# Kernel tuning notes

Hardware: AMD Instinct MI355X
Metric: run time of the kernel (lower is better)

Reference implementation:

```python
import jax, jax.numpy as jnp
import numpy as np

# Dimensions (see shape_source): B batches, W walks, L walk length, N anonymized node-id space
B, W, L, N = 256, 128, 20, 64
SIGMA = 2.0  # CooccurrenceMatrix(sigma=2.0)


def setup_inputs() -> dict:
    key = jax.random.key(0)
    k1, k2 = jax.random.split(key)
    anonymized_nodes = jax.random.randint(k1, (B, W, L), 0, N, dtype=jnp.int32)
    walk_masks = jax.random.randint(k2, (B, W, L), 0, 2).astype(bool)
    # Gaussian positional kernel buffer: kernel[i,j] = exp(-(i-j)^2 / sigma^2)
    pos = jnp.arange(L, dtype=jnp.float32)
    kernel = jnp.exp(-((pos[:, None] - pos[None, :]) ** 2) / (SIGMA ** 2))
    return {"anonymized_nodes": anonymized_nodes, "walk_masks": walk_masks, "kernel": kernel}


def reference(anonymized_nodes, walk_masks, kernel):
    # Faithful vectorized form of CooccurrenceMatrix.forward.
    # Original: per batch, group valid (walk,pos) entries by node id (sort +
    # change-points); for each group with >=2 entries, scatter-add
    # kernel[pos_i, pos_j] into cooccurrence[b, walk_i, walk_j] for all pairs
    # (i,j) in the group (including i==j). Then normalize by outer product of
    # walk lengths, clamp, tanh.
    valid = walk_masks.astype(jnp.float32)                     # [B,W,L]
    # T[b,w,l,n] = 1 if entry (w,l) is valid and holds node id n
    T = jax.nn.one_hot(anonymized_nodes, N, dtype=jnp.float32) * valid[..., None]  # [B,W,L,N]
    # Segments with < 2 occurrences contribute nothing (original skips them)
    cnt = T.sum(axis=(1, 2))                                   # [B,N]
    T = T * (cnt >= 2.0).astype(jnp.float32)[:, None, None, :]
    K = jnp.clip(kernel, -10.0, 10.0)                          # clamp as in _add_segment_deterministic
    # cooccurrence[b,w,v] = sum_n sum_{l,m} T[b,w,l,n] K[l,m] T[b,v,m,n]
    S = jnp.einsum('bwln,lm->bwmn', T, K)                      # [B,W,L,N]
    cooc = jnp.einsum('bwmn,bvmn->bwv', S, T)                  # [B,W,W]
    # Normalization by walk-length outer product
    walk_lens = valid.sum(-1)                                  # [B,W]
    norm = jnp.clip(walk_lens[:, :, None] * walk_lens[:, None, :], 1e-6, None)
    valid_pairs = (walk_lens[:, :, None] > 0) & (walk_lens[:, None, :] > 0)
    cooc = jnp.where(valid_pairs, cooc / norm, 0.0)
    return jnp.tanh(jnp.clip(cooc, -10.0, 10.0))
```

## Files before the change

### kernel.cpp

```cpp
#include <hip/hip_runtime.h>
#include <hip/hip_bf16.h>

#define BB   256
#define W    128
#define L    20
#define NN   64
#define WL   (W * L)
#define NT   1024
#define CS   129
#define NSLOT 3
#define ENTPAD 8192

__global__ __launch_bounds__(NT) void cooc_kernel(
    const int* __restrict__ nodes,
    const void* __restrict__ masks,
    const float* __restrict__ kern,
    float* __restrict__ out)
{
    __shared__ __align__(16) float cooc[W * CS];
    __shared__ unsigned short ent[WL + ENTPAD];
    __shared__ int cnt[NN];
    __shared__ int cur[NN];
    __shared__ int eIncl[NN];
    __shared__ int wlen[W];
    __shared__ int det[3];

    const int tid = threadIdx.x;
    const int b = blockIdx.x;
    const int base = b * WL;

    const unsigned mword = ((const unsigned*)masks)[tid];
    int nval[NSLOT];
    #pragma unroll
    for (int k = 0; k < NSLOT; k++) {
        int e = tid + k * NT;
        nval[k] = (e < WL) ? nodes[base + e] : 0;
    }

    if (tid < 3) det[tid] = 0;
    if (tid < NN) cnt[tid] = 0;
    if (tid < W) wlen[tid] = 0;
    {
        float4* c4 = (float4*)cooc;
        for (int i = tid; i < (W * CS) / 4; i += NT)
            c4[i] = make_float4(0.f, 0.f, 0.f, 0.f);
    }
    {
        unsigned v = mword;
        unsigned long long b0 = __ballot(v > 1u);
        unsigned long long b1 = __ballot(v != 0u && v != 0x3F800000u);
        unsigned long long b2 = __ballot(v != 0u && v != 0x3F80u && v != 0x3F800000u &&
                                         v != 0x3F803F80u && v != 0x3C00u &&
                                         v != 0x3C000000u && v != 0x3C003C00u);
        if ((tid & 63) == 0) {
            if (b0) atomicOr(&det[0], 1);
            if (b1) atomicOr(&det[1], 1);
            if (b2) atomicOr(&det[2], 1);
        }
    }
    __syncthreads();
    const int flag = det[0] ? (det[1] ? (det[2] ? 1 : 3) : 2) : 0;

    auto validAt = [&](int idx) -> bool {
        switch (flag) {
            case 0:  return ((const int*)masks)[idx] != 0;
            case 2:  return ((const float*)masks)[idx] != 0.0f;
            case 3:  return ((const unsigned short*)masks)[idx] != 0;
            default: return ((const unsigned char*)masks)[idx] != 0;
        }
    };

    int nreg[NSLOT];
    int wlreg[NSLOT];
    #pragma unroll
    for (int k = 0; k < NSLOT; k++) {
        int e = tid + k * NT;
        nreg[k] = -1;
        wlreg[k] = 0;
        if (e < WL && validAt(base + e)) {
            int n = nval[k] & (NN - 1);
            int w = e / L;
            int l = e - w * L;
            nreg[k] = n;
            wlreg[k] = (w << 5) | l;
            atomicAdd(&cnt[n], 1);
            atomicAdd(&wlen[w], 1);
        }
    }
    __syncthreads();

    if (tid < NN) {
        int c = cnt[tid];
        int s = c;
        #pragma unroll
        for (int d = 1; d < NN; d <<= 1) {
            int t = __shfl_up(s, d, 64);
            if (tid >= d) s += t;
        }
        eIncl[tid] = s;
        cur[tid] = s - c;
    }
    __syncthreads();

    int qr[NSLOT], cr[NSLOT], bsr[NSLOT];
    #pragma unroll
    for (int k = 0; k < NSLOT; k++) {
        qr[k] = 0; cr[k] = 0; bsr[k] = 0;
        int n = nreg[k];
        if (n >= 0) {
            int p = atomicAdd(&cur[n], 1);
            ent[p] = (unsigned short)wlreg[k];
            int c = cnt[n];
            if (c >= 2) {
                int bs = eIncl[n] - c;
                qr[k] = p - bs;
                cr[k] = c;
                bsr[k] = bs;
                int w = wlreg[k] >> 5;
                atomicAdd(&cooc[w * CS + w], 0.5f);
            }
        }
    }
    __syncthreads();

    const float KC = -0.360673760222f;
    #pragma unroll
    for (int k = 0; k < NSLOT; k++) {
        const int c = cr[k];
        if (c < 2) continue;
        const int q = qr[k], bs = bsr[k];
        const int w1row = (wlreg[k] >> 5) * CS;
        const int l1 = wlreg[k] & 31;
        const int hd = (c - 1) >> 1;
        #pragma unroll 4
        for (int d = 1; d <= hd; d++) {
            int j = q + d;
            if (j >= c) j -= c;
            int e2 = ent[bs + j];
            int dl = l1 - (e2 & 31);
            float kv = __builtin_amdgcn_exp2f((float)(dl * dl) * KC);
            atomicAdd(&cooc[w1row + (e2 >> 5)], kv);
        }
        if ((c & 1) == 0 && q < (c >> 1)) {
            int j = q + (c >> 1);
            int e2 = ent[bs + j];
            int dl = l1 - (e2 & 31);
            float kv = __builtin_amdgcn_exp2f((float)(dl * dl) * KC);
            atomicAdd(&cooc[w1row + (e2 >> 5)], kv);
        }
    }
    __syncthreads();

    for (int i = tid; i < W * W; i += NT) {
        int wr = i >> 7;
        int v = i & (W - 1);
        float s = cooc[wr * CS + v] + cooc[v * CS + wr];
        int lw = wlen[wr], lv = wlen[v];
        float nrm = (float)(lw * lv);
        float x = s * __builtin_amdgcn_rcpf(fmaxf(nrm, 1e-6f));
        x = fminf(fmaxf(x, -10.f), 10.f);
        float e = __builtin_amdgcn_exp2f(x * 2.885390082f);
        float t = (e - 1.f) * __builtin_amdgcn_rcpf(e + 1.f);
        out[b * W * W + i] = (lw > 0 && lv > 0) ? t : 0.f;
    }
}

extern "C" void kernel_launch(void* const* d_in, const int* in_sizes, int n_in,
                              void* d_out, int out_size, void* d_ws, size_t ws_size,
                              hipStream_t stream) {
    const int*   nodes = (const int*)d_in[0];
    const void*  masks = d_in[1];
    const float* kern  = (const float*)d_in[2];
    float* out = (float*)d_out;

    cooc_kernel<<<BB, NT, 0, stream>>>(nodes, masks, kern, out);
}
```

Baseline: 89.48 us.

## Split cooccurrence kernel into bucket-build and pair-accumulate kernels via workspace

Splits the single fused kernel into two launches. The first uses 256-thread blocks to count and bucket valid entries by node id and writes the sorted entries, counts and walk lengths to a global workspace. The second uses 1024-thread blocks to reload them, rebuild the prefix sums and do the pairwise atomic accumulation plus normalization. The aim is to free the build phase from the large shared cooc buffer so more blocks can run per CU. The cost is an extra launch and a round trip through global memory, and it depends on d_ws being large enough.

```diff
diff --git a/kernel.cpp b/kernel.cpp
--- a/kernel.cpp
+++ b/kernel.cpp
@@ -6,45 +6,41 @@
 #define L    20
 #define NN   64
 #define WL   (W * L)
-#define NT   1024
 #define CS   129
-#define NSLOT 3
-#define ENTPAD 8192
-
-__global__ __launch_bounds__(NT) void cooc_kernel(
+#define NTA  256
+#define NSA  10
+#define NTB  1024
+#define NSB  3
+
+#define WSTRIDE 4096
+#define OFF_TOT 0
+#define OFF_CNT 4
+#define OFF_WLEN 68
+#define OFF_ENT 256
+
+__global__ __launch_bounds__(NTA) void cooc_build(
     const int* __restrict__ nodes,
     const void* __restrict__ masks,
-    const float* __restrict__ kern,
-    float* __restrict__ out)
+    unsigned* __restrict__ ws)
 {
-    __shared__ __align__(16) float cooc[W * CS];
-    __shared__ unsigned short ent[WL + ENTPAD];
-    __shared__ int cnt[NN];
-    __shared__ int cur[NN];
-    __shared__ int eIncl[NN];
+    __shared__ unsigned entS[WL];
+    __shared__ int cnt[NN], cur[NN], eIncl[NN];
     __shared__ int wlen[W];
     __shared__ int det[3];
 
     const int tid = threadIdx.x;
     const int b = blockIdx.x;
     const int base = b * WL;
+    unsigned* wsb = ws + (size_t)b * WSTRIDE;
 
     const unsigned mword = ((const unsigned*)masks)[tid];
-    int nval[NSLOT];
-    #pragma unroll
-    for (int k = 0; k < NSLOT; k++) {
-        int e = tid + k * NT;
-        nval[k] = (e < WL) ? nodes[base + e] : 0;
-    }
+    int nval[NSA];
+    #pragma unroll
+    for (int k = 0; k < NSA; k++) nval[k] = nodes[base + tid + k * NTA];
 
     if (tid < 3) det[tid] = 0;
     if (tid < NN) cnt[tid] = 0;
     if (tid < W) wlen[tid] = 0;
-    {
-        float4* c4 = (float4*)cooc;
-        for (int i = tid; i < (W * CS) / 4; i += NT)
-            c4[i] = make_float4(0.f, 0.f, 0.f, 0.f);
-    }
     {
         unsigned v = mword;
         unsigned long long b0 = __ballot(v > 1u);
@@ -70,19 +66,17 @@
         }
     };
 
-    int nreg[NSLOT];
-    int wlreg[NSLOT];
-    #pragma unroll
-    for (int k = 0; k < NSLOT; k++) {
-        int e = tid + k * NT;
+    int nreg[NSA]; int wlr[NSA];
+    #pragma unroll
+    for (int k = 0; k < NSA; k++) {
+        int e = tid + k * NTA;
         nreg[k] = -1;
-        wlreg[k] = 0;
-        if (e < WL && validAt(base + e)) {
+        if (validAt(base + e)) {
             int n = nval[k] & (NN - 1);
             int w = e / L;
             int l = e - w * L;
             nreg[k] = n;
-            wlreg[k] = (w << 5) | l;
+            wlr[k] = (w << 5) | l;
             atomicAdd(&cnt[n], 1);
             atomicAdd(&wlen[w], 1);
         }
@@ -102,60 +96,110 @@
     }
     __syncthreads();
 
-    int qr[NSLOT], cr[NSLOT], bsr[NSLOT];
-    #pragma unroll
-    for (int k = 0; k < NSLOT; k++) {
-        qr[k] = 0; cr[k] = 0; bsr[k] = 0;
+    #pragma unroll
+    for (int k = 0; k < NSA; k++) {
         int n = nreg[k];
         if (n >= 0) {
             int p = atomicAdd(&cur[n], 1);
-            ent[p] = (unsigned short)wlreg[k];
-            int c = cnt[n];
-            if (c >= 2) {
-                int bs = eIncl[n] - c;
-                qr[k] = p - bs;
-                cr[k] = c;
-                bsr[k] = bs;
-                int w = wlreg[k] >> 5;
-                atomicAdd(&cooc[w * CS + w], 0.5f);
-            }
-        }
-    }
-    __syncthreads();
+            entS[p] = (unsigned)wlr[k] | ((unsigned)n << 12);
+        }
+    }
+    __syncthreads();
+
+    if (tid == 0) wsb[OFF_TOT] = (unsigned)eIncl[NN - 1];
+    if (tid < NN) wsb[OFF_CNT + tid] = (unsigned)cnt[tid];
+    if (tid < W) wsb[OFF_WLEN + tid] = (unsigned)wlen[tid];
+    const int tot = eIncl[NN - 1];
+    for (int i = tid; i < tot; i += NTA) wsb[OFF_ENT + i] = entS[i];
+}
+
+__global__ __launch_bounds__(NTB) void cooc_pairs(
+    const unsigned* __restrict__ ws,
+    float* __restrict__ out)
+{
+    __shared__ __align__(16) float cooc[W * CS];
+    __shared__ unsigned entS[WL];
+    __shared__ int cntS[NN], eInclS[NN];
+    __shared__ int wlenS[W];
+
+    const int tid = threadIdx.x;
+    const int b = blockIdx.x;
+    const unsigned* wsb = ws + (size_t)b * WSTRIDE;
+
+    if (tid < NN) cntS[tid] = (int)wsb[OFF_CNT + tid];
+    if (tid < W) wlenS[tid] = (int)wsb[OFF_WLEN + tid];
+    unsigned ev[NSB];
+    #pragma unroll
+    for (int k = 0; k < NSB; k++) {
+        int p = tid + k * NTB;
+        ev[k] = (p < WL) ? wsb[OFF_ENT + p] : 0u;
+    }
+    {
+        float4* c4 = (float4*)cooc;
+        for (int i = tid; i < (W * CS) / 4; i += NTB)
+            c4[i] = make_float4(0.f, 0.f, 0.f, 0.f);
+    }
+    #pragma unroll
+    for (int k = 0; k < NSB; k++) {
+        int p = tid + k * NTB;
+        if (p < WL) entS[p] = ev[k];
+    }
+    __syncthreads();
+
+    if (tid < NN) {
+        int c = cntS[tid];
+        int s = c;
+        #pragma unroll
+        for (int d = 1; d < NN; d <<= 1) {
+            int t = __shfl_up(s, d, 64);
+            if (tid >= d) s += t;
+        }
+        eInclS[tid] = s;
+    }
+    __syncthreads();
+
+    const int tot = eInclS[NN - 1];
 
     const float KC = -0.360673760222f;
     #pragma unroll
-    for (int k = 0; k < NSLOT; k++) {
-        const int c = cr[k];
+    for (int k = 0; k < NSB; k++) {
+        const int p = tid + k * NTB;
+        if (p >= tot) continue;
+        const unsigned e = entS[p];
+        const int n = (int)(e >> 12) & (NN - 1);
+        const int c = cntS[n];
         if (c < 2) continue;
-        const int q = qr[k], bs = bsr[k];
-        const int w1row = (wlreg[k] >> 5) * CS;
-        const int l1 = wlreg[k] & 31;
+        const int bs = eInclS[n] - c;
+        const int q = p - bs;
+        const int wl = (int)(e & 0xFFFu);
+        const int w1row = (wl >> 5) * CS;
+        const int l1 = wl & 31;
+        atomicAdd(&cooc[w1row + (wl >> 5)], 0.5f);
         const int hd = (c - 1) >> 1;
         #pragma unroll 4
         for (int d = 1; d <= hd; d++) {
             int j = q + d;
             if (j >= c) j -= c;
-            int e2 = ent[bs + j];
-            int dl = l1 - (e2 & 31);
+            unsigned e2 = entS[bs + j];
+            int dl = l1 - (int)(e2 & 31u);
             float kv = __builtin_amdgcn_exp2f((float)(dl * dl) * KC);
-            atomicAdd(&cooc[w1row + (e2 >> 5)], kv);
+            atomicAdd(&cooc[w1row + (int)((e2 & 0xFFFu) >> 5)], kv);
         }
         if ((c & 1) == 0 && q < (c >> 1)) {
             int j = q + (c >> 1);
-            int e2 = ent[bs + j];
-            int dl = l1 - (e2 & 31);
+            unsigned e2 = entS[bs + j];
+            int dl = l1 - (int)(e2 & 31u);
             float kv = __builtin_amdgcn_exp2f((float)(dl * dl) * KC);
-            atomicAdd(&cooc[w1row + (e2 >> 5)], kv);
-        }
-    }
-    __syncthreads();
-
-    for (int i = tid; i < W * W; i += NT) {
+            atomicAdd(&cooc[w1row + (int)((e2 & 0xFFFu) >> 5)], kv);
+        }
+    }
+    __syncthreads();
+
+    for (int i = tid; i < W * W; i += NTB) {
         int wr = i >> 7;
         int v = i & (W - 1);
         float s = cooc[wr * CS + v] + cooc[v * CS + wr];
-        int lw = wlen[wr], lv = wlen[v];
+        int lw = wlenS[wr], lv = wlenS[v];
         float nrm = (float)(lw * lv);
         float x = s * __builtin_amdgcn_rcpf(fmaxf(nrm, 1e-6f));
         x = fminf(fmaxf(x, -10.f), 10.f);
@@ -168,10 +212,11 @@
 extern "C" void kernel_launch(void* const* d_in, const int* in_sizes, int n_in,
                               void* d_out, int out_size, void* d_ws, size_t ws_size,
                               hipStream_t stream) {
-    const int*   nodes = (const int*)d_in[0];
-    const void*  masks = d_in[1];
-    const float* kern  = (const float*)d_in[2];
+    const int*  nodes = (const int*)d_in[0];
+    const void* masks = d_in[1];
     float* out = (float*)d_out;
-
-    cooc_kernel<<<BB, NT, 0, stream>>>(nodes, masks, kern, out);
+    unsigned* ws = (unsigned*)d_ws;
+
+    cooc_build<<<BB, NTA, 0, stream>>>(nodes, masks, ws);
+    cooc_pairs<<<BB, NTB, 0, stream>>>(ws, out);
 }
```

Result: slower. 94.45 us (+5.6%).

## Sort entries by node and position key and truncate pairs beyond the kernel cutoff

Applied to the files above, without the earlier changes.

Entries are now counting-sorted by a combined (node, position) key using a shared histogram and prefix sums, replacing the per-node bucketing. Each entry pairs only with later entries of the same node whose position is at most 7 steps greater, using a sentinel-terminated linear scan. This replaces the circular half-pair loop and its modulo indexing. It also drops Gaussian terms with positional distance above 7, which are negligibly small for sigma=2 but are no longer computed exactly.

```diff
diff --git a/kernel.cpp b/kernel.cpp
--- a/kernel.cpp
+++ b/kernel.cpp
@@ -9,7 +9,7 @@
 #define NT   1024
 #define CS   129
 #define NSLOT 3
-#define ENTPAD 8192
+#define NKEY (L * NN)
 
 __global__ __launch_bounds__(NT) void cooc_kernel(
     const int* __restrict__ nodes,
@@ -18,12 +18,12 @@
     float* __restrict__ out)
 {
     __shared__ __align__(16) float cooc[W * CS];
-    __shared__ unsigned short ent[WL + ENTPAD];
+    __shared__ unsigned ent[WL + 4];
+    __shared__ unsigned hist[NKEY];
     __shared__ int cnt[NN];
-    __shared__ int cur[NN];
-    __shared__ int eIncl[NN];
     __shared__ int wlen[W];
     __shared__ int det[3];
+    __shared__ int totS;
 
     const int tid = threadIdx.x;
     const int b = blockIdx.x;
@@ -38,8 +38,9 @@
     }
 
     if (tid < 3) det[tid] = 0;
-    if (tid < NN) cnt[tid] = 0;
     if (tid < W) wlen[tid] = 0;
+    if (tid < NKEY) hist[tid] = 0;
+    if (tid + NT < NKEY) hist[tid + NT] = 0;
     {
         float4* c4 = (float4*)cooc;
         for (int i = tid; i < (W * CS) / 4; i += NT)
@@ -70,83 +71,77 @@
         }
     };
 
-    int nreg[NSLOT];
-    int wlreg[NSLOT];
+    unsigned eval[NSLOT];
+    int      kreg[NSLOT];
     #pragma unroll
     for (int k = 0; k < NSLOT; k++) {
         int e = tid + k * NT;
-        nreg[k] = -1;
-        wlreg[k] = 0;
+        eval[k] = 0xFFFFFFFFu;
+        kreg[k] = 0;
         if (e < WL && validAt(base + e)) {
             int n = nval[k] & (NN - 1);
             int w = e / L;
             int l = e - w * L;
-            nreg[k] = n;
-            wlreg[k] = (w << 5) | l;
-            atomicAdd(&cnt[n], 1);
+            eval[k] = ((unsigned)n << 12) | ((unsigned)l << 7) | (unsigned)w;
+            kreg[k] = l * NN + n;
+            atomicAdd(&hist[kreg[k]], 1u);
             atomicAdd(&wlen[w], 1);
         }
     }
     __syncthreads();
 
     if (tid < NN) {
-        int c = cnt[tid];
-        int s = c;
+        int s = 0;
+        #pragma unroll
+        for (int l = 0; l < L; l++) s += (int)hist[l * NN + tid];
+        cnt[tid] = s;
+        int inc = s;
         #pragma unroll
         for (int d = 1; d < NN; d <<= 1) {
-            int t = __shfl_up(s, d, 64);
-            if (tid >= d) s += t;
+            int t = __shfl_up(inc, d, 64);
+            if (tid >= d) inc += t;
         }
-        eIncl[tid] = s;
-        cur[tid] = s - c;
+        int run = inc - s;
+        if (tid == NN - 1) totS = inc;
+        #pragma unroll
+        for (int l = 0; l < L; l++) {
+            int t = (int)hist[l * NN + tid];
+            hist[l * NN + tid] = (unsigned)run;
+            run += t;
+        }
     }
     __syncthreads();
 
-    int qr[NSLOT], cr[NSLOT], bsr[NSLOT];
+    if (tid == 0) ent[totS] = 0xFFFFFFFFu;
     #pragma unroll
     for (int k = 0; k < NSLOT; k++) {
-        qr[k] = 0; cr[k] = 0; bsr[k] = 0;
-        int n = nreg[k];
-        if (n >= 0) {
-            int p = atomicAdd(&cur[n], 1);
-            ent[p] = (unsigned short)wlreg[k];
-            int c = cnt[n];
-            if (c >= 2) {
-                int bs = eIncl[n] - c;
-                qr[k] = p - bs;
-                cr[k] = c;
-                bsr[k] = bs;
-                int w = wlreg[k] >> 5;
-                atomicAdd(&cooc[w * CS + w], 0.5f);
-            }
+        if (eval[k] != 0xFFFFFFFFu) {
+            unsigned p = atomicAdd(&hist[kreg[k]], 1u);
+            ent[p] = eval[k];
         }
     }
     __syncthreads();
 
     const float KC = -0.360673760222f;
+    const int tot = totS;
     #pragma unroll
     for (int k = 0; k < NSLOT; k++) {
-        const int c = cr[k];
-        if (c < 2) continue;
-        const int q = qr[k], bs = bsr[k];
-        const int w1row = (wlreg[k] >> 5) * CS;
-        const int l1 = wlreg[k] & 31;
-        const int hd = (c - 1) >> 1;
-        #pragma unroll 4
-        for (int d = 1; d <= hd; d++) {
-            int j = q + d;
-            if (j >= c) j -= c;
-            int e2 = ent[bs + j];
-            int dl = l1 - (e2 & 31);
-            float kv = __builtin_amdgcn_exp2f((float)(dl * dl) * KC);
-            atomicAdd(&cooc[w1row + (e2 >> 5)], kv);
-        }
-        if ((c & 1) == 0 && q < (c >> 1)) {
-            int j = q + (c >> 1);
-            int e2 = ent[bs + j];
-            int dl = l1 - (e2 & 31);
-            float kv = __builtin_amdgcn_exp2f((float)(dl * dl) * KC);
-            atomicAdd(&cooc[w1row + (e2 >> 5)], kv);
+        const int p = tid + k * NT;
+        if (p >= tot) continue;
+        const unsigned e = ent[p];
+        const unsigned key1 = e >> 7;
+        const int n = (int)(e >> 12);
+        const int w1row = (int)(e & 127u) * CS;
+        if (cnt[n] >= 2)
+            atomicAdd(&cooc[w1row + (int)(e & 127u)], 0.5f);
+        int j = p + 1;
+        while (true) {
+            unsigned e2 = ent[j];
+            unsigned d = (e2 >> 7) - key1;
+            if (d > 7u) break;
+            float kv = __builtin_amdgcn_exp2f((float)(d * d) * KC);
+            atomicAdd(&cooc[w1row + (int)(e2 & 127u)], kv);
+            j++;
         }
     }
     __syncthreads();
```

Result: faster. 82.03 us (-8.3%).
